# Kernel optimization log

Hardware: AMD Instinct MI355X
Metric: run time of the kernel (lower is better)

Reference implementation:

```python
import jax, jax.numpy as jnp
import numpy as np

B, N, D, G = 32, 1024, 512, 32  # batch, set size, in_features, num_gaussians


def setup_inputs() -> dict:
    key = jax.random.key(0)
    k1, k2 = jax.random.split(key)
    minibatch = jax.random.normal(k1, (B, N, D), dtype=jnp.float32)
    # xavier_uniform for Linear(D -> G)
    limit = float(np.sqrt(6.0 / (D + G)))
    W_pi = jax.random.uniform(k2, (G, D), dtype=jnp.float32, minval=-limit, maxval=limit)
    b_pi = jnp.zeros((G,), dtype=jnp.float32)
    return {"minibatch": minibatch, "W_pi": W_pi, "b_pi": b_pi}


def reference(minibatch, W_pi, b_pi):
    d = minibatch.shape[-1]
    o = d // 2
    # mixture weights per (batch, sample): softmax over gaussian axis
    logits = jnp.einsum('bnd,gd->bng', minibatch, W_pi) + b_pi  # [B,N,G]
    pi = jax.nn.softmax(logits, axis=2)
    mu = minibatch[:, :, :o]        # [B,N,O]
    sigma = minibatch[:, :, -o:]    # [B,N,O]
    weights = jnp.mean(pi, axis=1)  # [B,G]
    denom = jnp.sum(pi, axis=1)     # [B,G]
    # weighted first moment -> locs (vectorized over all gaussians at once)
    m1 = jnp.einsum('bng,bno->bgo', pi, mu)                 # [B,G,O]
    locs = m1 / denom[:, :, None]                            # [B,G,O]
    # weighted E[mu^2 + sigma^2]; variance = E[mu^2+sigma^2] - locs^2
    # (identical math to sum(pi*((locs-mu)^2 + sigma^2))/sum(pi))
    m2 = jnp.einsum('bng,bno->bgo', pi, mu * mu + sigma * sigma)
    var = m2 / denom[:, :, None] - locs * locs
    scales = jnp.sqrt(jnp.maximum(var, 0.0))                 # [B,G,O]
    return weights, scales, locs
```

## Files before the change

kernel.cpp:

```cpp
#include <hip/hip_runtime.h>
#include <stdint.h>

#define B_ 32
#define N_ 1024
#define D_ 512
#define G_ 32

typedef __attribute__((ext_vector_type(8))) short short8;
typedef __attribute__((ext_vector_type(4))) float f32x4;
union U4S8 { uint4 u; short8 s; };

#define WS_DN  4194304
#define WS_WF  4202496

__device__ inline uint32_t pack_bf16x2(float a, float b) {
  uint32_t ua = __float_as_uint(a);
  uint32_t ub = __float_as_uint(b);
  ua += 0x7FFFu + ((ua >> 16) & 1u);
  ub += 0x7FFFu + ((ub >> 16) & 1u);
  return (ua >> 16) | (ub & 0xFFFF0000u);
}
__device__ inline uint16_t bf16r(float a) {
  uint32_t u = __float_as_uint(a);
  u += 0x7FFFu + ((u >> 16) & 1u);
  return (uint16_t)(u >> 16);
}
__device__ inline float bflo(uint32_t u) { return __uint_as_float(u << 16); }
__device__ inline float bfhi(uint32_t u) { return __uint_as_float(u & 0xFFFF0000u); }
__device__ inline int slot_of(int o) { return (o & 7) ^ ((o >> 3) & 3); }

__global__ __launch_bounds__(256) void mdn_k0(
    const float* __restrict__ W, float* ws)
{
  int s = blockIdx.x * 256 + threadIdx.x;
  int g = s >> 6;
  int d0 = (s & 63) * 8;
  const float4* src = (const float4*)(W + g * D_ + d0);
  float4 f0 = src[0], f1 = src[1];
  int ks = d0 >> 5, ksub = (d0 >> 3) & 3;
  uint4 v;
  v.x = pack_bf16x2(f0.x, f0.y); v.y = pack_bf16x2(f0.z, f0.w);
  v.z = pack_bf16x2(f1.x, f1.y); v.w = pack_bf16x2(f1.z, f1.w);
  ((uint4*)(ws + WS_WF))[(ks * 4 + ksub) * 32 + g] = v;
}

__global__ __launch_bounds__(512, 2) void mdn_kf(
    const float* __restrict__ x, const float* __restrict__ bpi, float* ws)
{
  __shared__ uint32_t XTmu[16384];
  __shared__ uint32_t XTsg[16384];
  __shared__ uint32_t PT[2048];
  __shared__ float wpart[8][32];

  const int t = threadIdx.x;
  const int bid = blockIdx.x;
  const int b = bid >> 3;
  const int n0 = (bid & 7) * 128;
  const int w = t >> 6;
  const int lane = t & 63;
  const int l15 = lane & 15, l4 = lane >> 4;

  const float* abase =
      x + ((size_t)(b * N_ + n0 + w * 16 + l15)) * D_ + l4 * 8;
  const uint4* wf4 = (const uint4*)(ws + WS_WF);
  const int r = w * 16 + l15;

  f32x4 acc0 = {0.f, 0.f, 0.f, 0.f};
  f32x4 acc1 = {0.f, 0.f, 0.f, 0.f};

  #pragma unroll
  for (int h = 0; h < 2; ++h) {
    float4 fa[8], fb[8];
    #pragma unroll
    for (int k = 0; k < 8; ++k) {
      const float* s = abase + (h * 8 + k) * 32;
      fa[k] = *(const float4*)s; fb[k] = *(const float4*)(s + 4);
    }
    uint16_t* a16 = (uint16_t*)(h ? XTsg : XTmu);
    #pragma unroll
    for (int k = 0; k < 8; ++k) {
      int ks = h * 8 + k;
      uint32_t ua[4];
      ua[0] = pack_bf16x2(fa[k].x, fa[k].y);
      ua[1] = pack_bf16x2(fa[k].z, fa[k].w);
      ua[2] = pack_bf16x2(fb[k].x, fb[k].y);
      ua[3] = pack_bf16x2(fb[k].z, fb[k].w);
      int ob = l4 * 8 + k * 32;
      #pragma unroll
      for (int i = 0; i < 4; ++i) {
        int o0 = ob + 2 * i, o1 = o0 + 1;
        a16[o0 * 128 + (r ^ (slot_of(o0) << 3))] = (uint16_t)ua[i];
        a16[o1 * 128 + (r ^ (slot_of(o1) << 3))] = (uint16_t)(ua[i] >> 16);
      }
      U4S8 a; a.u.x = ua[0]; a.u.y = ua[1]; a.u.z = ua[2]; a.u.w = ua[3];
      int wi = (ks * 4 + l4) * 32 + l15;
      U4S8 w0, w1;
      w0.u = wf4[wi];
      w1.u = wf4[wi + 16];
      acc0 = __builtin_amdgcn_mfma_f32_16x16x32_bf16(a.s, w0.s, acc0, 0, 0, 0);
      acc1 = __builtin_amdgcn_mfma_f32_16x16x32_bf16(a.s, w1.s, acc1, 0, 0, 0);
    }
  }

  float bs0 = bpi[l15], bs1 = bpi[16 + l15];
  float pi0[4], pi1[4];
  float dsum0 = 0.f, dsum1 = 0.f;
  #pragma unroll
  for (int j = 0; j < 4; ++j) {
    float v0 = acc0[j] + bs0, v1 = acc1[j] + bs1;
    float m = fmaxf(v0, v1);
    m = fmaxf(m, __shfl_xor(m, 1));
    m = fmaxf(m, __shfl_xor(m, 2));
    m = fmaxf(m, __shfl_xor(m, 4));
    m = fmaxf(m, __shfl_xor(m, 8));
    float e0 = __expf(v0 - m), e1 = __expf(v1 - m);
    float s = e0 + e1;
    s += __shfl_xor(s, 1); s += __shfl_xor(s, 2);
    s += __shfl_xor(s, 4); s += __shfl_xor(s, 8);
    float inv = 1.0f / s;
    pi0[j] = e0 * inv; pi1[j] = e1 * inv;
    dsum0 += pi0[j];   dsum1 += pi1[j];
  }
  dsum0 += __shfl_xor(dsum0, 16); dsum0 += __shfl_xor(dsum0, 32);
  dsum1 += __shfl_xor(dsum1, 16); dsum1 += __shfl_xor(dsum1, 32);
  if (lane < 16) { wpart[w][lane] = dsum0; wpart[w][16 + lane] = dsum1; }

  {
    uint16_t* p16 = (uint16_t*)PT;
    int rbase = w * 16 + l4 * 4;
    int g0 = l15, g1 = 16 + l15;
    int s0 = slot_of(g0) << 3, s1 = slot_of(g1) << 3;
    #pragma unroll
    for (int j = 0; j < 4; ++j) {
      int rr = rbase + j;
      p16[g0 * 128 + (rr ^ s0)] = bf16r(pi0[j]);
      p16[g1 * 128 + (rr ^ s1)] = bf16r(pi1[j]);
    }
  }
  __syncthreads();

  if (t < 32) {
    float s = 0.f;
    #pragma unroll
    for (int ww = 0; ww < 8; ++ww) s += wpart[ww][t];
    ws[WS_DN + (size_t)bid * 32 + t] = s;
  }

  f32x4 m1a[2][2] = {{{0.f,0.f,0.f,0.f},{0.f,0.f,0.f,0.f}},
                     {{0.f,0.f,0.f,0.f},{0.f,0.f,0.f,0.f}}};
  f32x4 m2a[2][2] = {{{0.f,0.f,0.f,0.f},{0.f,0.f,0.f,0.f}},
                     {{0.f,0.f,0.f,0.f},{0.f,0.f,0.f,0.f}}};
  const int gA0 = l15, gA1 = 16 + l15;
  const int sA0 = slot_of(gA0) << 2, sA1 = slot_of(gA1) << 2;

  #pragma unroll
  for (int ks = 0; ks < 4; ++ks) {
    int rofs = ks * 16 + l4 * 4;
    U4S8 a0, a1;
    a0.u = *(const uint4*)(PT + gA0 * 64 + (rofs ^ sA0));
    a1.u = *(const uint4*)(PT + gA1 * 64 + (rofs ^ sA1));
    #pragma unroll
    for (int ot = 0; ot < 2; ++ot) {
      int o = w * 32 + ot * 16 + l15;
      int idx = o * 64 + (rofs ^ (slot_of(o) << 2));
      U4S8 Bm; Bm.u = *(const uint4*)(XTmu + idx);
      uint4 sg4 = *(const uint4*)(XTsg + idx);
      uint32_t bm[4] = {Bm.u.x, Bm.u.y, Bm.u.z, Bm.u.w};
      uint32_t sw[4] = {sg4.x, sg4.y, sg4.z, sg4.w};
      U4S8 B2;
      uint32_t b2w[4];
      #pragma unroll
      for (int i = 0; i < 4; ++i) {
        float lo = bflo(bm[i]) * bflo(bm[i]) + bflo(sw[i]) * bflo(sw[i]);
        float hi = bfhi(bm[i]) * bfhi(bm[i]) + bfhi(sw[i]) * bfhi(sw[i]);
        b2w[i] = pack_bf16x2(lo, hi);
      }
      B2.u.x = b2w[0]; B2.u.y = b2w[1]; B2.u.z = b2w[2]; B2.u.w = b2w[3];
      m1a[0][ot] = __builtin_amdgcn_mfma_f32_16x16x32_bf16(a0.s, Bm.s, m1a[0][ot], 0, 0, 0);
      m1a[1][ot] = __builtin_amdgcn_mfma_f32_16x16x32_bf16(a1.s, Bm.s, m1a[1][ot], 0, 0, 0);
      m2a[0][ot] = __builtin_amdgcn_mfma_f32_16x16x32_bf16(a0.s, B2.s, m2a[0][ot], 0, 0, 0);
      m2a[1][ot] = __builtin_amdgcn_mfma_f32_16x16x32_bf16(a1.s, B2.s, m2a[1][ot], 0, 0, 0);
    }
  }

  float* dst = ws + (size_t)bid * 16384;
  #pragma unroll
  for (int gt = 0; gt < 2; ++gt) {
    #pragma unroll
    for (int ot = 0; ot < 2; ++ot) {
      int col = w * 32 + ot * 16 + l15;
      #pragma unroll
      for (int jj = 0; jj < 4; ++jj) {
        int g = gt * 16 + l4 * 4 + jj;
        dst[g * 512 + col] = m1a[gt][ot][jj];
        dst[g * 512 + 256 + col] = m2a[gt][ot][jj];
      }
    }
  }
}

__global__ __launch_bounds__(256) void mdn_k3(
    const float* __restrict__ ws, float* __restrict__ out)
{
  __shared__ float dnm[G_];
  const int blk = blockIdx.x;
  const int b = blk >> 3, oc = blk & 7;
  const int t = threadIdx.x;
  if (t < G_) {
    float s = 0.f;
    #pragma unroll
    for (int c = 0; c < 8; ++c) s += ws[WS_DN + (size_t)(b * 8 + c) * 32 + t];
    dnm[t] = s;
    if (oc == 0) out[b * G_ + t] = s * (1.0f / 1024.0f);
  }
  __syncthreads();
  const int g = t >> 3;
  const int o = oc * 32 + (t & 7) * 4;
  float4 m1 = make_float4(0.f, 0.f, 0.f, 0.f);
  float4 m2 = make_float4(0.f, 0.f, 0.f, 0.f);
  #pragma unroll
  for (int c = 0; c < 8; ++c) {
    const float* p = ws + (size_t)(b * 8 + c) * 16384 + g * 512;
    float4 a = *(const float4*)(p + o);
    float4 c2 = *(const float4*)(p + 256 + o);
    m1.x += a.x; m1.y += a.y; m1.z += a.z; m1.w += a.w;
    m2.x += c2.x; m2.y += c2.y; m2.z += c2.z; m2.w += c2.w;
  }
  float inv = 1.0f / dnm[g];
  float4 lc = make_float4(m1.x * inv, m1.y * inv, m1.z * inv, m1.w * inv);
  float4 sc;
  sc.x = sqrtf(fmaxf(m2.x * inv - lc.x * lc.x, 0.f));
  sc.y = sqrtf(fmaxf(m2.y * inv - lc.y * lc.y, 0.f));
  sc.z = sqrtf(fmaxf(m2.z * inv - lc.z * lc.z, 0.f));
  sc.w = sqrtf(fmaxf(m2.w * inv - lc.w * lc.w, 0.f));
  float* scales = out + 1024;
  float* locs = out + 1024 + 262144;
  int oi = ((b * G_ + g) << 8) + o;
  *(float4*)(scales + oi) = sc;
  *(float4*)(locs + oi) = lc;
}

extern "C" void kernel_launch(void* const* d_in, const int* in_sizes, int n_in,
                              void* d_out, int out_size, void* d_ws, size_t ws_size,
                              hipStream_t stream)
{
  const float* x = (const float*)d_in[0];
  const float* W = (const float*)d_in[1];
  const float* bpi = (const float*)d_in[2];
  float* out = (float*)d_out;
  float* ws = (float*)d_ws;
  hipLaunchKernelGGL(mdn_k0, dim3(8), dim3(256), 0, stream, W, ws);
  hipLaunchKernelGGL(mdn_kf, dim3(256), dim3(512), 0, stream, x, bpi, ws);
  hipLaunchKernelGGL(mdn_k3, dim3(256), dim3(256), 0, stream, ws, out);
}
```

Baseline: 31.47 us.

## Store X tile row-major in LDS and read transposed via ds_read_b64_tr_b16

Result: no change. 31.81 us (+1.1%).

```diff
diff --git a/kernel.cpp b/kernel.cpp
--- a/kernel.cpp
+++ b/kernel.cpp
@@ -47,8 +47,7 @@
 __global__ __launch_bounds__(512, 2) void mdn_kf(
     const float* __restrict__ x, const float* __restrict__ bpi, float* ws)
 {
-  __shared__ uint32_t XTmu[16384];
-  __shared__ uint32_t XTsg[16384];
+  __shared__ uint32_t XT[32768];
   __shared__ uint32_t PT[2048];
   __shared__ float wpart[8][32];
 
@@ -76,23 +75,19 @@
       const float* s = abase + (h * 8 + k) * 32;
       fa[k] = *(const float4*)s; fb[k] = *(const float4*)(s + 4);
     }
-    uint16_t* a16 = (uint16_t*)(h ? XTsg : XTmu);
     #pragma unroll
     for (int k = 0; k < 8; ++k) {
       int ks = h * 8 + k;
-      uint32_t ua[4];
-      ua[0] = pack_bf16x2(fa[k].x, fa[k].y);
-      ua[1] = pack_bf16x2(fa[k].z, fa[k].w);
-      ua[2] = pack_bf16x2(fb[k].x, fb[k].y);
-      ua[3] = pack_bf16x2(fb[k].z, fb[k].w);
-      int ob = l4 * 8 + k * 32;
-      #pragma unroll
-      for (int i = 0; i < 4; ++i) {
-        int o0 = ob + 2 * i, o1 = o0 + 1;
-        a16[o0 * 128 + (r ^ (slot_of(o0) << 3))] = (uint16_t)ua[i];
-        a16[o1 * 128 + (r ^ (slot_of(o1) << 3))] = (uint16_t)(ua[i] >> 16);
+      U4S8 a;
+      a.u.x = pack_bf16x2(fa[k].x, fa[k].y);
+      a.u.y = pack_bf16x2(fa[k].z, fa[k].w);
+      a.u.z = pack_bf16x2(fb[k].x, fb[k].y);
+      a.u.w = pack_bf16x2(fb[k].z, fb[k].w);
+      {
+        int d0 = l4 * 8 + ks * 32;
+        unsigned xtb = (unsigned)((d0 >> 4) * 4096 + r * 32 + (d0 & 15) * 2);
+        *(uint4*)((char*)XT + xtb) = a.u;
       }
-      U4S8 a; a.u.x = ua[0]; a.u.y = ua[1]; a.u.z = ua[2]; a.u.w = ua[3];
       int wi = (ks * 4 + l4) * 32 + l15;
       U4S8 w0, w1;
       w0.u = wf4[wi];
@@ -152,21 +147,33 @@
                      {{0.f,0.f,0.f,0.f},{0.f,0.f,0.f,0.f}}};
   const int gA0 = l15, gA1 = 16 + l15;
   const int sA0 = slot_of(gA0) << 2, sA1 = slot_of(gA1) << 2;
-
-  #pragma unroll
-  for (int ks = 0; ks < 4; ++ks) {
-    int rofs = ks * 16 + l4 * 4;
+  const unsigned xtb0 = (unsigned)(uintptr_t)XT;
+
+  #pragma unroll
+  for (int ksi = 0; ksi < 4; ++ksi) {
+    int rofs = ksi * 16 + l4 * 4;
     U4S8 a0, a1;
     a0.u = *(const uint4*)(PT + gA0 * 64 + (rofs ^ sA0));
     a1.u = *(const uint4*)(PT + gA1 * 64 + (rofs ^ sA1));
+    const unsigned rowb = (unsigned)(ksi * 1024 + l4 * 256 + l15 * 8);
     #pragma unroll
     for (int ot = 0; ot < 2; ++ot) {
-      int o = w * 32 + ot * 16 + l15;
-      int idx = o * 64 + (rofs ^ (slot_of(o) << 2));
-      U4S8 Bm; Bm.u = *(const uint4*)(XTmu + idx);
-      uint4 sg4 = *(const uint4*)(XTsg + idx);
+      unsigned am = xtb0 + (unsigned)((w * 2 + ot) * 4096) + rowb;
+      unsigned as = am + 16 * 4096;
+      uint64_t q0, q1, q2, q3;
+      asm volatile("ds_read_b64_tr_b16 %0, %1" : "=v"(q0) : "v"(am));
+      asm volatile("ds_read_b64_tr_b16 %0, %1 offset:128" : "=v"(q1) : "v"(am));
+      asm volatile("ds_read_b64_tr_b16 %0, %1" : "=v"(q2) : "v"(as));
+      asm volatile("ds_read_b64_tr_b16 %0, %1 offset:128" : "=v"(q3) : "v"(as));
+      asm volatile("s_waitcnt lgkmcnt(0)" ::: "memory");
+      __builtin_amdgcn_sched_barrier(0);
+      U4S8 Bm, Bs;
+      Bm.u.x = (uint32_t)q0; Bm.u.y = (uint32_t)(q0 >> 32);
+      Bm.u.z = (uint32_t)q1; Bm.u.w = (uint32_t)(q1 >> 32);
+      Bs.u.x = (uint32_t)q2; Bs.u.y = (uint32_t)(q2 >> 32);
+      Bs.u.z = (uint32_t)q3; Bs.u.w = (uint32_t)(q3 >> 32);
       uint32_t bm[4] = {Bm.u.x, Bm.u.y, Bm.u.z, Bm.u.w};
-      uint32_t sw[4] = {sg4.x, sg4.y, sg4.z, sg4.w};
+      uint32_t sw[4] = {Bs.u.x, Bs.u.y, Bs.u.z, Bs.u.w};
       U4S8 B2;
       uint32_t b2w[4];
       #pragma unroll
```
